# Kernel optimization log

Hardware: AMD Instinct MI355X
Metric: run time of the kernel (lower is better)

Reference implementation:

```python
import jax, jax.numpy as jnp
import numpy as np

B, S, E, H = 8, 2048, 512, 8
HD = E // H
N_IND = 64


def setup_inputs() -> dict:
    key = jax.random.key(0)
    ks = jax.random.split(key, 10)
    s = 1.0 / np.sqrt(E)
    return {
        "x": jax.random.normal(ks[0], (B, S, E), jnp.float32),
        "Wq": jax.random.normal(ks[1], (E, E), jnp.float32) * s,
        "bq": jax.random.normal(ks[2], (E,), jnp.float32) * s,
        "Wk": jax.random.normal(ks[3], (E, E), jnp.float32) * s,
        "bk": jax.random.normal(ks[4], (E,), jnp.float32) * s,
        "Wv": jax.random.normal(ks[5], (E, E), jnp.float32) * s,
        "bv": jax.random.normal(ks[6], (E,), jnp.float32) * s,
        "Wo": jax.random.normal(ks[7], (E, E), jnp.float32) * s,
        "bo": jax.random.normal(ks[8], (E,), jnp.float32) * s,
        "industry_ids": jax.random.randint(ks[9], (S,), 0, N_IND, jnp.int32),
    }


def reference(x, Wq, bq, Wk, bk, Wv, bv, Wo, bo, industry_ids):
    # same-industry block mask [S, S]; every row attends at least to itself
    mask = industry_ids[:, None] == industry_ids[None, :]
    # projections (torch Linear: y = x @ W.T + b)
    q = (x @ Wq.T + bq).reshape(B, S, H, HD).transpose(0, 2, 1, 3)  # [B,H,S,HD]
    k = (x @ Wk.T + bk).reshape(B, S, H, HD).transpose(0, 2, 1, 3)
    v = (x @ Wv.T + bv).reshape(B, S, H, HD).transpose(0, 2, 1, 3)
    scores = jnp.einsum("bhqd,bhkd->bhqk", q, k) / np.sqrt(HD).astype(jnp.float32)
    scores = jnp.where(mask[None, None, :, :], scores, -jnp.inf)
    attn = jax.nn.softmax(scores, axis=-1)  # dropout is identity at inference
    out = jnp.einsum("bhqk,bhkd->bhqd", attn, v)
    out = out.transpose(0, 2, 1, 3).reshape(B, S, E)
    return out @ Wo.T + bo
```

## Files before the change

### kernel.cpp

```cpp
#include <hip/hip_runtime.h>
#include <cstdint>

#define DEVFN __device__ __forceinline__

typedef __bf16 bf16x8 __attribute__((ext_vector_type(8)));
typedef float f32x4 __attribute__((ext_vector_type(4)));
typedef unsigned int uint;

constexpr int Bc = 8, Sc = 2048, Ec = 512, Hc = 8, HDc = 64, NI = 64;
constexpr int Mtot = Bc * Sc;
constexpr int Kdim = Ec;
constexpr int MAXITEMS = 128;

DEVFN unsigned short f2bf(float f) {
  unsigned u = __builtin_bit_cast(unsigned, f);
  u += 0x7fffu + ((u >> 16) & 1u);
  return (unsigned short)(u >> 16);
}

typedef const void __attribute__((address_space(1))) gvoid_t;
typedef void __attribute__((address_space(3))) lvoid_t;
DEVFN void gload16(const void* g, void* l) {
  __builtin_amdgcn_global_load_lds((gvoid_t*)g, (lvoid_t*)l, 16, 0, 0);
}

DEVFN uint cvtpk(float lo, float hi) {
  uint r;
  asm("v_cvt_pk_bf16_f32 %0, %1, %2" : "=v"(r) : "v"(lo), "v"(hi));
  return r;
}

#define WAIT_VM_BARRIER(N)                                            \
  do {                                                                \
    asm volatile("s_waitcnt vmcnt(" #N ")\n\ts_barrier" ::: "memory"); \
    __builtin_amdgcn_sched_barrier(0);                                \
  } while (0)
#define WAIT_LGKM_BARRIER()                                            \
  do {                                                                 \
    asm volatile("s_waitcnt lgkmcnt(0)\n\ts_barrier" ::: "memory");    \
    __builtin_amdgcn_sched_barrier(0);                                 \
  } while (0)

__global__ void cvt_x_kernel(const float* __restrict__ x, const int* __restrict__ perm,
                             ushort* __restrict__ xb) {
  int i = blockIdx.x * 256 + threadIdx.x;
  int mp = i >> 7;
  int c = i & 127;
  int b = mp >> 11, p = mp & (Sc - 1);
  int srow = (b << 11) | perm[p];
  float4 v = *(const float4*)(x + (size_t)srow * Ec + c * 4);
  ushort4 o = {f2bf(v.x), f2bf(v.y), f2bf(v.z), f2bf(v.w)};
  ((ushort4*)xb)[i] = o;
}

__global__ void cvt_w_kernel(const float* __restrict__ Wq, const float* __restrict__ Wk,
                             const float* __restrict__ Wv, const float* __restrict__ Wo,
                             ushort* __restrict__ Wcat, ushort* __restrict__ Wob) {
  int i = blockIdx.x * 256 + threadIdx.x;
  int idx = i * 4;
  int n = idx >> 9, k = idx & 511;
  const float* src;
  ushort* dst;
  if (n < 512)       { src = Wq + (size_t)n * 512 + k;          dst = Wcat + (size_t)n * 512 + k; }
  else if (n < 1024) { src = Wk + (size_t)(n - 512) * 512 + k;  dst = Wcat + (size_t)n * 512 + k; }
  else if (n < 1536) { src = Wv + (size_t)(n - 1024) * 512 + k; dst = Wcat + (size_t)n * 512 + k; }
  else               { src = Wo + (size_t)(n - 1536) * 512 + k; dst = Wob + (size_t)(n - 1536) * 512 + k; }
  float4 v = *(const float4*)src;
  ushort4 o = {f2bf(v.x), f2bf(v.y), f2bf(v.z), f2bf(v.w)};
  *(ushort4*)dst = o;
}

__global__ void sort_kernel(const int* __restrict__ ids, int* __restrict__ perm,
                            int* __restrict__ gstart, int* __restrict__ gsz,
                            int* __restrict__ items, int* __restrict__ nitems) {
  __shared__ int sid[Sc];
  __shared__ int hist[NI];
  __shared__ int base[NI];
  int t = threadIdx.x;
  if (t < NI) hist[t] = 0;
  for (int i = t; i < Sc; i += 256) sid[i] = ids[i];
  __syncthreads();
  for (int i = t; i < Sc; i += 256) atomicAdd(&hist[sid[i]], 1);
  __syncthreads();
  if (t == 0) {
    int run = 0;
    for (int g = 0; g < NI; ++g) { base[g] = run; run += hist[g]; }
    int cnt = 0;
    for (int g = 0; g < NI; ++g)
      for (int q0 = 0; q0 < hist[g]; q0 += 32) items[cnt++] = (g << 16) | q0;
    *nitems = cnt;
  }
  __syncthreads();
  if (t < NI) { gstart[t] = base[t]; gsz[t] = hist[t]; }
  int lane = t & 63, w = t >> 6;
  for (int g = w; g < NI; g += 4) {
    int run = base[g];
    for (int c = 0; c < Sc; c += 64) {
      int tok = c + lane;
      int id = sid[tok];
      unsigned long long mask = __ballot(id == g);
      if (id == g) {
        int rank = __popcll(mask & ((1ull << lane) - 1ull));
        perm[run + rank] = tok;
      }
      run += __popcll(mask);
    }
  }
}

__global__ __launch_bounds__(512) void gemm_qkv256(
    const ushort* __restrict__ A, const ushort* __restrict__ Bw,
    const float* __restrict__ bias0, const float* __restrict__ bias1,
    const float* __restrict__ bias2, ushort* __restrict__ qkvout) {
  constexpr int NK = Kdim / 64;
  __shared__ __align__(16) char ldsraw[131072];
  ushort* sAb = (ushort*)ldsraw;
  ushort* sBb = (ushort*)(ldsraw + 65536);
  const int tid = threadIdx.x;
  const int lane = tid & 63;
  const int wave = tid >> 6;
  const int wm = wave >> 2;
  const int wn = wave & 3;
  const int orig = blockIdx.x;
  const int xcd = orig & 7, gl = orig >> 3;
  const int mbase = (xcd * 8 + (gl & 7)) * 256;
  const int nbase = (gl >> 3) * 256;

  f32x4 acc[8][4] = {};

  const int rowS = tid >> 3;
  const int kc = tid & 7;

  auto stage = [&](int buf, int kt) {
    const int k0 = kt * 64;
#pragma unroll
    for (int c = 0; c < 4; ++c) {
      int row = rowS + c * 64;
      int kcp = (kc ^ (row & 7)) * 8;
      gload16(A + (size_t)(mbase + row) * Kdim + k0 + kcp,
              sAb + buf * 16384 + (wave * 64 + c * 512) * 8);
      gload16(Bw + (size_t)(nbase + row) * Kdim + k0 + kcp,
              sBb + buf * 16384 + (wave * 64 + c * 512) * 8);
    }
  };

  stage(0, 0);
  stage(1, 1);

  for (int kt = 0; kt < NK; ++kt) {
    const int cur = kt & 1;
    if (kt < NK - 1) {
      WAIT_VM_BARRIER(8);
    } else {
      WAIT_VM_BARRIER(0);
    }

    const char* Ab = (const char*)(sAb + cur * 16384);
    const char* Bb = (const char*)(sBb + cur * 16384);
    __builtin_amdgcn_s_setprio(1);
#pragma unroll
    for (int kk = 0; kk < 2; ++kk) {
      bf16x8 af[8], bfv[4];
#pragma unroll
      for (int i = 0; i < 8; ++i) {
        int row = wm * 128 + i * 16 + (lane & 15);
        int off = row * 128 + kk * 64 + (lane >> 4) * 16;
        off ^= (row & 7) << 4;
        af[i] = *(const bf16x8*)(Ab + off);
      }
#pragma unroll
      for (int j = 0; j < 4; ++j) {
        int col = wn * 64 + j * 16 + (lane & 15);
        int off = col * 128 + kk * 64 + (lane >> 4) * 16;
        off ^= (col & 7) << 4;
        bfv[j] = *(const bf16x8*)(Bb + off);
      }
#pragma unroll
      for (int i = 0; i < 8; ++i)
#pragma unroll
        for (int j = 0; j < 4; ++j)
          acc[i][j] = __builtin_amdgcn_mfma_f32_16x16x32_bf16(af[i], bfv[j], acc[i][j], 0, 0, 0);
    }
    __builtin_amdgcn_s_setprio(0);

    WAIT_LGKM_BARRIER();
    if (kt + 2 < NK) stage(cur, kt + 2);
  }

  {
    ushort* T = (ushort*)ldsraw;
#pragma unroll
    for (int i = 0; i < 8; ++i) {
#pragma unroll
      for (int j = 0; j < 4; ++j) {
        int nl = wn * 64 + j * 16 + (lane & 15);
        int n = nbase + nl;
        float bv = (n < 512) ? bias0[n] : (n < 1024) ? bias1[n - 512] : bias2[n - 1024];
#pragma unroll
        for (int r = 0; r < 4; ++r) {
          int ml = wm * 128 + i * 16 + (lane >> 4) * 4 + r;
          T[ml * 256 + nl] = f2bf(acc[i][j][r] + bv);
        }
      }
    }
    __syncthreads();
#pragma unroll
    for (int k = 0; k < 16; ++k) {
      int c = tid + 512 * k;
      int row = c >> 5, col8 = (c & 31) * 8;
      uint4 w = *(const uint4*)(T + row * 256 + col8);
      int n0 = nbase + col8;
      int proj = n0 >> 9, h = (n0 >> 6) & 7, d0 = n0 & 63;
      int p = mbase + row;
      int bidx = p >> 11, pl = p & (Sc - 1);
      size_t off = (size_t)proj * ((size_t)Bc * Hc * Sc * HDc) +
                   (size_t)((bidx * Hc + h) * Sc + pl) * HDc + d0;
      *(uint4*)(qkvout + off) = w;
    }
  }
}

__global__ __launch_bounds__(256) void gemm_out128(
    const ushort* __restrict__ A, const ushort* __restrict__ Bw,
    const float* __restrict__ bias0, const int* __restrict__ permarg,
    float* __restrict__ out) {
  constexpr int NK = Kdim / 64;
  constexpr int NTOT = 512;
  __shared__ __align__(16) char ldsraw[65536];
  ushort* sAb = (ushort*)ldsraw;
  ushort* sBb = (ushort*)(ldsraw + 32768);
  const int tid = threadIdx.x;
  const int lane = tid & 63;
  const int wave = tid >> 6;
  const int wr = wave >> 1, wc = wave & 1;
  const int orig = blockIdx.x;
  const int xcd = orig & 7, gl = orig >> 3;
  const int mbase = (xcd * 16 + (gl & 15)) * 128;
  const int nbase = (gl >> 4) * 128;

  f32x4 acc[4][4] = {};

  const int rowS = wave * 32 + (lane >> 3);
  const int kc = lane & 7;

  auto stage = [&](int buf, int kt) {
    const int k0 = kt * 64;
#pragma unroll
    for (int c = 0; c < 4; ++c) {
      int row = rowS + c * 8;
      int kcp = (kc ^ (row & 7)) * 8;
      gload16(A + (size_t)(mbase + row) * Kdim + k0 + kcp,
              sAb + buf * 8192 + (wave * 256 + c * 64) * 8);
      gload16(Bw + (size_t)(nbase + row) * Kdim + k0 + kcp,
              sBb + buf * 8192 + (wave * 256 + c * 64) * 8);
    }
  };

  stage(0, 0);
  stage(1, 1);

  for (int kt = 0; kt < NK; ++kt) {
    const int cur = kt & 1;
    if (kt < NK - 1) {
      WAIT_VM_BARRIER(8);
    } else {
      WAIT_VM_BARRIER(0);
    }

    const char* Ab = (const char*)(sAb + cur * 8192);
    const char* Bb = (const char*)(sBb + cur * 8192);
    __builtin_amdgcn_s_setprio(1);
#pragma unroll
    for (int kk = 0; kk < 2; ++kk) {
      bf16x8 af[4], bfv[4];
#pragma unroll
      for (int i = 0; i < 4; ++i) {
        int row = wr * 64 + i * 16 + (lane & 15);
        int off = row * 128 + kk * 64 + (lane >> 4) * 16;
        off ^= (row & 7) << 4;
        af[i] = *(const bf16x8*)(Ab + off);
      }
#pragma unroll
      for (int j = 0; j < 4; ++j) {
        int col = wc * 64 + j * 16 + (lane & 15);
        int off = col * 128 + kk * 64 + (lane >> 4) * 16;
        off ^= (col & 7) << 4;
        bfv[j] = *(const bf16x8*)(Bb + off);
      }
#pragma unroll
      for (int i = 0; i < 4; ++i)
#pragma unroll
        for (int j = 0; j < 4; ++j)
          acc[i][j] = __builtin_amdgcn_mfma_f32_16x16x32_bf16(af[i], bfv[j], acc[i][j], 0, 0, 0);
    }
    __builtin_amdgcn_s_setprio(0);

    WAIT_LGKM_BARRIER();
    if (kt + 2 < NK) stage(cur, kt + 2);
  }

  float* T = (float*)ldsraw;
#pragma unroll
  for (int i = 0; i < 4; ++i) {
#pragma unroll
    for (int j = 0; j < 4; ++j) {
      int nl = wc * 64 + j * 16 + (lane & 15);
      float bv = bias0[nbase + nl];
#pragma unroll
      for (int r = 0; r < 4; ++r) {
        int ml = wr * 64 + i * 16 + (lane >> 4) * 4 + r;
        T[ml * 128 + nl] = acc[i][j][r] + bv;
      }
    }
  }
  __syncthreads();
#pragma unroll
  for (int k = 0; k < 16; ++k) {
    int c = tid + 256 * k;
    int row = c >> 5, col4 = (c & 31) * 4;
    float4 w = *(const float4*)(T + row * 128 + col4);
    int p = mbase + row;
    int bidx = p >> 11;
    int orow = (bidx << 11) | permarg[p & (Sc - 1)];
    *(float4*)(out + (size_t)orow * NTOT + nbase + col4) = w;
  }
}

__global__ __launch_bounds__(64) void attn5_kernel(
    const ushort* __restrict__ qkv, const int* __restrict__ gstart,
    const int* __restrict__ gsz, const int* __restrict__ items,
    const int* __restrict__ nitems, ushort* __restrict__ obuf) {
  __shared__ __align__(16) ushort vt[64 * 40];
  if ((int)blockIdx.x >= *nitems) return;
  const int iv = items[blockIdx.x];
  const int g = iv >> 16, q0 = iv & 0xffff;
  const int bh = blockIdx.y;
  const int start = gstart[g], n = gsz[g];
  const int lane = threadIdx.x;
  const int ql = lane & 15, lg = lane >> 4;

  const size_t planeSz = (size_t)Bc * Hc * Sc * HDc;
  const ushort* qb = qkv + (size_t)bh * Sc * HDc;
  const ushort* kb = qb + planeSz;
  const ushort* vb = kb + planeSz;

  bf16x8 qf[2][2];
#pragma unroll
  for (int qt = 0; qt < 2; ++qt) {
    int row = min(start + q0 + qt * 16 + ql, Sc - 1);
#pragma unroll
    for (int h = 0; h < 2; ++h)
      qf[qt][h] = *(const bf16x8*)(qb + (size_t)row * HDc + h * 32 + lg * 8);
  }

  f32x4 oacc[2][4] = {};
  float lsum[2] = {0.f, 0.f};

  const int vk = lane & 31;
  const int vh = (lane >> 5) * 32;
  const int Lbase = 4 * (ql + 32 * (lg & 1));

  const int npair = (n + 31) >> 5;
  for (int pr = 0; pr < npair; ++pr) {
    const int c0 = pr * 32;
    int vrow = min(start + c0 + vk, Sc - 1);
    const uint4* vp = (const uint4*)(vb + (size_t)vrow * HDc + vh);
    uint4 v0 = vp[0], v1 = vp[1], v2 = vp[2], v3 = vp[3];

    bf16x8 kf[2][2];
#pragma unroll
    for (int t = 0; t < 2; ++t) {
      int row = min(start + c0 + t * 16 + ql, Sc - 1);
#pragma unroll
      for (int h = 0; h < 2; ++h)
        kf[t][h] = *(const bf16x8*)(kb + (size_t)row * HDc + h * 32 + lg * 8);
    }

    uint pw[2][4];
#pragma unroll
    for (int qt = 0; qt < 2; ++qt) {
      f32x4 s0 = {}, s1 = {};
      s0 = __builtin_amdgcn_mfma_f32_16x16x32_bf16(kf[0][0], qf[qt][0], s0, 0, 0, 0);
      s0 = __builtin_amdgcn_mfma_f32_16x16x32_bf16(kf[0][1], qf[qt][1], s0, 0, 0, 0);
      s1 = __builtin_amdgcn_mfma_f32_16x16x32_bf16(kf[1][0], qf[qt][0], s1, 0, 0, 0);
      s1 = __builtin_amdgcn_mfma_f32_16x16x32_bf16(kf[1][1], qf[qt][1], s1, 0, 0, 0);
      float p0[4], p1[4];
      float ls = 0.f;
#pragma unroll
      for (int r = 0; r < 4; ++r) {
        int kk = c0 + 4 * lg + r;
        float e0 = (kk < n) ? __expf(s0[r] * 0.125f) : 0.f;
        float e1 = (kk + 16 < n) ? __expf(s1[r] * 0.125f) : 0.f;
        p0[r] = e0;
        p1[r] = e1;
        ls += e0 + e1;
      }
      lsum[qt] += ls;
      uint a0 = cvtpk(p0[0], p0[1]), b0 = cvtpk(p0[2], p0[3]);
      uint a1 = cvtpk(p1[0], p1[1]), b1 = cvtpk(p1[2], p1[3]);
      uint pA0 = __builtin_amdgcn_ds_bpermute(Lbase, a0);
      uint pB0 = __builtin_amdgcn_ds_bpermute(Lbase, b0);
      uint pA1 = __builtin_amdgcn_ds_bpermute(Lbase, a1);
      uint pB1 = __builtin_amdgcn_ds_bpermute(Lbase, b1);
      uint pC0 = __builtin_amdgcn_ds_bpermute(Lbase + 64, a0);
      uint pD0 = __builtin_amdgcn_ds_bpermute(Lbase + 64, b0);
      uint pC1 = __builtin_amdgcn_ds_bpermute(Lbase + 64, a1);
      uint pD1 = __builtin_amdgcn_ds_bpermute(Lbase + 64, b1);
      bool t0 = lg < 2;
      pw[qt][0] = t0 ? pA0 : pA1;
      pw[qt][1] = t0 ? pB0 : pB1;
      pw[qt][2] = t0 ? pC0 : pC1;
      pw[qt][3] = t0 ? pD0 : pD1;
    }

    {
      uint w[16] = {v0.x, v0.y, v0.z, v0.w, v1.x, v1.y, v1.z, v1.w,
                    v2.x, v2.y, v2.z, v2.w, v3.x, v3.y, v3.z, v3.w};
#pragma unroll
      for (int i = 0; i < 16; ++i) {
        vt[(vh + 2 * i) * 40 + vk] = (ushort)(w[i] & 0xffffu);
        vt[(vh + 2 * i + 1) * 40 + vk] = (ushort)(w[i] >> 16);
      }
    }
    asm volatile("s_waitcnt lgkmcnt(0)" ::: "memory");
    __builtin_amdgcn_sched_barrier(0);
    bf16x8 vf[4];
#pragma unroll
    for (int dq = 0; dq < 4; ++dq)
      vf[dq] = *(const bf16x8*)(vt + (dq * 16 + ql) * 40 + lg * 8);
    asm volatile("s_waitcnt lgkmcnt(0)" ::: "memory");
    __builtin_amdgcn_sched_barrier(0);
#pragma unroll
    for (int qt = 0; qt < 2; ++qt) {
      union { uint u[4]; bf16x8 v; } pf;
      pf.u[0] = pw[qt][0]; pf.u[1] = pw[qt][1]; pf.u[2] = pw[qt][2]; pf.u[3] = pw[qt][3];
#pragma unroll
      for (int dq = 0; dq < 4; ++dq)
        oacc[qt][dq] = __builtin_amdgcn_mfma_f32_16x16x32_bf16(vf[dq], pf.v, oacc[qt][dq], 0, 0, 0);
    }
  }

#pragma unroll
  for (int qt = 0; qt < 2; ++qt) {
    float l = lsum[qt];
    l += __shfl_xor(l, 16);
    l += __shfl_xor(l, 32);
    float inv = 1.f / l;
    int qi = q0 + qt * 16 + ql;
    if (qi < n) {
      int p = start + qi;
      ushort* op = obuf + (size_t)((bh >> 3) * Sc + p) * Ec + (bh & 7) * HDc + lg * 4;
#pragma unroll
      for (int dq = 0; dq < 4; ++dq) {
        uint w0 = cvtpk(oacc[qt][dq][0] * inv, oacc[qt][dq][1] * inv);
        uint w1 = cvtpk(oacc[qt][dq][2] * inv, oacc[qt][dq][3] * inv);
        uint2 wv = {w0, w1};
        *(uint2*)(op + dq * 16) = wv;
      }
    }
  }
}

extern "C" void kernel_launch(void* const* d_in, const int* in_sizes, int n_in,
                              void* d_out, int out_size, void* d_ws, size_t ws_size,
                              hipStream_t stream) {
  const float* x  = (const float*)d_in[0];
  const float* Wq = (const float*)d_in[1];
  const float* bq = (const float*)d_in[2];
  const float* Wk = (const float*)d_in[3];
  const float* bk = (const float*)d_in[4];
  const float* Wv = (const float*)d_in[5];
  const float* bv = (const float*)d_in[6];
  const float* Wo = (const float*)d_in[7];
  const float* bo = (const float*)d_in[8];
  const int* ids  = (const int*)d_in[9];
  float* out = (float*)d_out;

  char* ws = (char*)d_ws;
  ushort* xb   = (ushort*)(ws);
  ushort* Wcat = (ushort*)(ws + 16777216);
  ushort* Wob  = (ushort*)(ws + 18350080);
  ushort* qkv  = (ushort*)(ws + 18874368);
  ushort* obuf = (ushort*)(ws + 69206016);
  int* perm    = (int*)(ws + 85983232);
  int* gstart  = perm + Sc;
  int* gsz     = gstart + NI;
  int* items   = gsz + NI;
  int* nitems  = items + MAXITEMS;

  sort_kernel<<<dim3(1), dim3(256), 0, stream>>>(ids, perm, gstart, gsz, items, nitems);
  cvt_x_kernel<<<dim3(Mtot * Ec / 4 / 256), dim3(256), 0, stream>>>(x, perm, xb);
  cvt_w_kernel<<<dim3(2048 * 512 / 4 / 256), dim3(256), 0, stream>>>(Wq, Wk, Wv, Wo, Wcat, Wob);
  gemm_qkv256<<<dim3(Mtot / 256 * 6), dim3(512), 0, stream>>>(xb, Wcat, bq, bk, bv, qkv);
  attn5_kernel<<<dim3(MAXITEMS, Bc * Hc), dim3(64), 0, stream>>>(qkv, gstart, gsz, items,
                                                                 nitems, obuf);
  gemm_out128<<<dim3(Mtot / 128 * 4), dim3(256), 0, stream>>>(obuf, Wob, bo, perm, out);
}
```

Before: 134.5 us.

## Merge sort and weight conversion into one launch; shrink QKV GEMM tile to 128

```diff
diff --git a/kernel.cpp b/kernel.cpp
--- a/kernel.cpp
+++ b/kernel.cpp
@@ -41,6 +41,62 @@
     __builtin_amdgcn_sched_barrier(0);                                 \
   } while (0)
 
+__global__ void prep_kernel(const int* __restrict__ ids, int* __restrict__ perm,
+                            int* __restrict__ gstart, int* __restrict__ gsz,
+                            int* __restrict__ items, int* __restrict__ nitems,
+                            const float* __restrict__ Wq, const float* __restrict__ Wk,
+                            const float* __restrict__ Wv, const float* __restrict__ Wo,
+                            ushort* __restrict__ Wcat, ushort* __restrict__ Wob) {
+  if (blockIdx.x == 0) {
+    __shared__ int sid[Sc];
+    __shared__ int hist[NI];
+    __shared__ int base[NI];
+    int t = threadIdx.x;
+    if (t < NI) hist[t] = 0;
+    for (int i = t; i < Sc; i += 256) sid[i] = ids[i];
+    __syncthreads();
+    for (int i = t; i < Sc; i += 256) atomicAdd(&hist[sid[i]], 1);
+    __syncthreads();
+    if (t == 0) {
+      int run = 0;
+      for (int g = 0; g < NI; ++g) { base[g] = run; run += hist[g]; }
+      int cnt = 0;
+      for (int g = 0; g < NI; ++g)
+        for (int q0 = 0; q0 < hist[g]; q0 += 32) items[cnt++] = (g << 16) | q0;
+      *nitems = cnt;
+    }
+    __syncthreads();
+    if (t < NI) { gstart[t] = base[t]; gsz[t] = hist[t]; }
+    int lane = t & 63, w = t >> 6;
+    for (int g = w; g < NI; g += 4) {
+      int run = base[g];
+      for (int c = 0; c < Sc; c += 64) {
+        int tok = c + lane;
+        int id = sid[tok];
+        unsigned long long mask = __ballot(id == g);
+        if (id == g) {
+          int rank = __popcll(mask & ((1ull << lane) - 1ull));
+          perm[run + rank] = tok;
+        }
+        run += __popcll(mask);
+      }
+    }
+  } else {
+    int i = (blockIdx.x - 1) * 256 + threadIdx.x;
+    int idx = i * 4;
+    int n = idx >> 9, k = idx & 511;
+    const float* src;
+    ushort* dst;
+    if (n < 512)       { src = Wq + (size_t)n * 512 + k;          dst = Wcat + (size_t)n * 512 + k; }
+    else if (n < 1024) { src = Wk + (size_t)(n - 512) * 512 + k;  dst = Wcat + (size_t)n * 512 + k; }
+    else if (n < 1536) { src = Wv + (size_t)(n - 1024) * 512 + k; dst = Wcat + (size_t)n * 512 + k; }
+    else               { src = Wo + (size_t)(n - 1536) * 512 + k; dst = Wob + (size_t)(n - 1536) * 512 + k; }
+    float4 v = *(const float4*)src;
+    ushort4 o = {f2bf(v.x), f2bf(v.y), f2bf(v.z), f2bf(v.w)};
+    *(ushort4*)dst = o;
+  }
+}
+
 __global__ void cvt_x_kernel(const float* __restrict__ x, const int* __restrict__ perm,
                              ushort* __restrict__ xb) {
   int i = blockIdx.x * 256 + threadIdx.x;
@@ -53,94 +109,38 @@
   ((ushort4*)xb)[i] = o;
 }
 
-__global__ void cvt_w_kernel(const float* __restrict__ Wq, const float* __restrict__ Wk,
-                             const float* __restrict__ Wv, const float* __restrict__ Wo,
-                             ushort* __restrict__ Wcat, ushort* __restrict__ Wob) {
-  int i = blockIdx.x * 256 + threadIdx.x;
-  int idx = i * 4;
-  int n = idx >> 9, k = idx & 511;
-  const float* src;
-  ushort* dst;
-  if (n < 512)       { src = Wq + (size_t)n * 512 + k;          dst = Wcat + (size_t)n * 512 + k; }
-  else if (n < 1024) { src = Wk + (size_t)(n - 512) * 512 + k;  dst = Wcat + (size_t)n * 512 + k; }
-  else if (n < 1536) { src = Wv + (size_t)(n - 1024) * 512 + k; dst = Wcat + (size_t)n * 512 + k; }
-  else               { src = Wo + (size_t)(n - 1536) * 512 + k; dst = Wob + (size_t)(n - 1536) * 512 + k; }
-  float4 v = *(const float4*)src;
-  ushort4 o = {f2bf(v.x), f2bf(v.y), f2bf(v.z), f2bf(v.w)};
-  *(ushort4*)dst = o;
-}
-
-__global__ void sort_kernel(const int* __restrict__ ids, int* __restrict__ perm,
-                            int* __restrict__ gstart, int* __restrict__ gsz,
-                            int* __restrict__ items, int* __restrict__ nitems) {
-  __shared__ int sid[Sc];
-  __shared__ int hist[NI];
-  __shared__ int base[NI];
-  int t = threadIdx.x;
-  if (t < NI) hist[t] = 0;
-  for (int i = t; i < Sc; i += 256) sid[i] = ids[i];
-  __syncthreads();
-  for (int i = t; i < Sc; i += 256) atomicAdd(&hist[sid[i]], 1);
-  __syncthreads();
-  if (t == 0) {
-    int run = 0;
-    for (int g = 0; g < NI; ++g) { base[g] = run; run += hist[g]; }
-    int cnt = 0;
-    for (int g = 0; g < NI; ++g)
-      for (int q0 = 0; q0 < hist[g]; q0 += 32) items[cnt++] = (g << 16) | q0;
-    *nitems = cnt;
-  }
-  __syncthreads();
-  if (t < NI) { gstart[t] = base[t]; gsz[t] = hist[t]; }
-  int lane = t & 63, w = t >> 6;
-  for (int g = w; g < NI; g += 4) {
-    int run = base[g];
-    for (int c = 0; c < Sc; c += 64) {
-      int tok = c + lane;
-      int id = sid[tok];
-      unsigned long long mask = __ballot(id == g);
-      if (id == g) {
-        int rank = __popcll(mask & ((1ull << lane) - 1ull));
-        perm[run + rank] = tok;
-      }
-      run += __popcll(mask);
-    }
-  }
-}
-
-__global__ __launch_bounds__(512) void gemm_qkv256(
+__global__ __launch_bounds__(256) void gemm_qkv128(
     const ushort* __restrict__ A, const ushort* __restrict__ Bw,
     const float* __restrict__ bias0, const float* __restrict__ bias1,
     const float* __restrict__ bias2, ushort* __restrict__ qkvout) {
   constexpr int NK = Kdim / 64;
-  __shared__ __align__(16) char ldsraw[131072];
+  __shared__ __align__(16) char ldsraw[65536];
   ushort* sAb = (ushort*)ldsraw;
-  ushort* sBb = (ushort*)(ldsraw + 65536);
+  ushort* sBb = (ushort*)(ldsraw + 32768);
   const int tid = threadIdx.x;
   const int lane = tid & 63;
   const int wave = tid >> 6;
-  const int wm = wave >> 2;
-  const int wn = wave & 3;
+  const int wr = wave >> 1, wc = wave & 1;
   const int orig = blockIdx.x;
   const int xcd = orig & 7, gl = orig >> 3;
-  const int mbase = (xcd * 8 + (gl & 7)) * 256;
-  const int nbase = (gl >> 3) * 256;
-
-  f32x4 acc[8][4] = {};
-
-  const int rowS = tid >> 3;
-  const int kc = tid & 7;
+  const int mbase = (xcd * 16 + (gl & 15)) * 128;
+  const int nbase = (gl >> 4) * 128;
+
+  f32x4 acc[4][4] = {};
+
+  const int rowS = wave * 32 + (lane >> 3);
+  const int kc = lane & 7;
 
   auto stage = [&](int buf, int kt) {
     const int k0 = kt * 64;
 #pragma unroll
     for (int c = 0; c < 4; ++c) {
-      int row = rowS + c * 64;
+      int row = rowS + c * 8;
       int kcp = (kc ^ (row & 7)) * 8;
       gload16(A + (size_t)(mbase + row) * Kdim + k0 + kcp,
-              sAb + buf * 16384 + (wave * 64 + c * 512) * 8);
+              sAb + buf * 8192 + (wave * 256 + c * 64) * 8);
       gload16(Bw + (size_t)(nbase + row) * Kdim + k0 + kcp,
-              sBb + buf * 16384 + (wave * 64 + c * 512) * 8);
+              sBb + buf * 8192 + (wave * 256 + c * 64) * 8);
     }
   };
 
@@ -155,28 +155,28 @@
       WAIT_VM_BARRIER(0);
     }
 
-    const char* Ab = (const char*)(sAb + cur * 16384);
-    const char* Bb = (const char*)(sBb + cur * 16384);
+    const char* Ab = (const char*)(sAb + cur * 8192);
+    const char* Bb = (const char*)(sBb + cur * 8192);
     __builtin_amdgcn_s_setprio(1);
 #pragma unroll
     for (int kk = 0; kk < 2; ++kk) {
-      bf16x8 af[8], bfv[4];
-#pragma unroll
-      for (int i = 0; i < 8; ++i) {
-        int row = wm * 128 + i * 16 + (lane & 15);
+      bf16x8 af[4], bfv[4];
+#pragma unroll
+      for (int i = 0; i < 4; ++i) {
+        int row = wr * 64 + i * 16 + (lane & 15);
         int off = row * 128 + kk * 64 + (lane >> 4) * 16;
         off ^= (row & 7) << 4;
         af[i] = *(const bf16x8*)(Ab + off);
       }
 #pragma unroll
       for (int j = 0; j < 4; ++j) {
-        int col = wn * 64 + j * 16 + (lane & 15);
+        int col = wc * 64 + j * 16 + (lane & 15);
         int off = col * 128 + kk * 64 + (lane >> 4) * 16;
         off ^= (col & 7) << 4;
         bfv[j] = *(const bf16x8*)(Bb + off);
       }
 #pragma unroll
-      for (int i = 0; i < 8; ++i)
+      for (int i = 0; i < 4; ++i)
 #pragma unroll
         for (int j = 0; j < 4; ++j)
           acc[i][j] = __builtin_amdgcn_mfma_f32_16x16x32_bf16(af[i], bfv[j], acc[i][j], 0, 0, 0);
@@ -190,25 +190,25 @@
   {
     ushort* T = (ushort*)ldsraw;
 #pragma unroll
-    for (int i = 0; i < 8; ++i) {
+    for (int i = 0; i < 4; ++i) {
 #pragma unroll
       for (int j = 0; j < 4; ++j) {
-        int nl = wn * 64 + j * 16 + (lane & 15);
+        int nl = wc * 64 + j * 16 + (lane & 15);
         int n = nbase + nl;
         float bv = (n < 512) ? bias0[n] : (n < 1024) ? bias1[n - 512] : bias2[n - 1024];
 #pragma unroll
         for (int r = 0; r < 4; ++r) {
-          int ml = wm * 128 + i * 16 + (lane >> 4) * 4 + r;
-          T[ml * 256 + nl] = f2bf(acc[i][j][r] + bv);
+          int ml = wr * 64 + i * 16 + (lane >> 4) * 4 + r;
+          T[ml * 136 + nl] = f2bf(acc[i][j][r] + bv);
         }
       }
     }
     __syncthreads();
 #pragma unroll
-    for (int k = 0; k < 16; ++k) {
-      int c = tid + 512 * k;
-      int row = c >> 5, col8 = (c & 31) * 8;
-      uint4 w = *(const uint4*)(T + row * 256 + col8);
+    for (int k = 0; k < 8; ++k) {
+      int c = tid + 256 * k;
+      int row = c >> 4, col8 = (c & 15) * 8;
+      uint4 w = *(const uint4*)(T + row * 136 + col8);
       int n0 = nbase + col8;
       int proj = n0 >> 9, h = (n0 >> 6) & 7, d0 = n0 & 63;
       int p = mbase + row;
@@ -488,10 +488,10 @@
   int* items   = gsz + NI;
   int* nitems  = items + MAXITEMS;
 
-  sort_kernel<<<dim3(1), dim3(256), 0, stream>>>(ids, perm, gstart, gsz, items, nitems);
+  prep_kernel<<<dim3(1 + 2048 * 512 / 4 / 256), dim3(256), 0, stream>>>(
+      ids, perm, gstart, gsz, items, nitems, Wq, Wk, Wv, Wo, Wcat, Wob);
   cvt_x_kernel<<<dim3(Mtot * Ec / 4 / 256), dim3(256), 0, stream>>>(x, perm, xb);
-  cvt_w_kernel<<<dim3(2048 * 512 / 4 / 256), dim3(256), 0, stream>>>(Wq, Wk, Wv, Wo, Wcat, Wob);
-  gemm_qkv256<<<dim3(Mtot / 256 * 6), dim3(512), 0, stream>>>(xb, Wcat, bq, bk, bv, qkv);
+  gemm_qkv128<<<dim3(Mtot / 128 * 12), dim3(256), 0, stream>>>(xb, Wcat, bq, bk, bv, qkv);
   attn5_kernel<<<dim3(MAXITEMS, Bc * Hc), dim3(64), 0, stream>>>(qkv, gstart, gsz, items,
                                                                  nitems, obuf);
   gemm_out128<<<dim3(Mtot / 128 * 4), dim3(256), 0, stream>>>(obuf, Wob, bo, perm, out);
```

Measured after the change: 127.5 us. 1.06x faster.
